# Kernel optimization log

Hardware: AMD Instinct MI355X
Metric: run time of the kernel (lower is better)

The kernel has to match this reference:

```python
import jax, jax.numpy as jnp
import numpy as np

NUM_NODES = 100000
NUM_CLASS = 63  # output channels = num_class + 1 = 64
NUM_EDGES = 1600000


def setup_inputs() -> dict:
    key = jax.random.key(0)
    k1, k2, k3, k4 = jax.random.split(key, 4)
    edges = jax.random.randint(k1, (NUM_EDGES, 2), 0, NUM_NODES, dtype=jnp.int64 if jax.config.jax_enable_x64 else jnp.int32)
    weights = jax.random.uniform(k2, (NUM_EDGES,), dtype=jnp.float32)
    poss_edge = jax.random.uniform(k3, (NUM_EDGES, NUM_CLASS + 1), dtype=jnp.float32)
    # neighbour degree sums; keep away from zero for numerical sanity
    neighbours_sum = jax.random.uniform(k4, (NUM_NODES, 1), dtype=jnp.float32, minval=0.5, maxval=1.5)
    return {"edges": edges, "weights": weights, "poss_edge": poss_edge, "neighbours_sum": neighbours_sum}


def reference(edges, weights, poss_edge, neighbours_sum):
    # value = poss_edge * weights[:, None]  -> [E, C+1]
    value = poss_edge * weights[:, None]
    # scatter_add over src node index (edges[:, 0]) into [N, C+1]
    src = edges[:, 0]
    poss_node = jax.ops.segment_sum(value, src, num_segments=NUM_NODES)
    # normalize per node by neighbour weight sum ([N,1] broadcast)
    poss_node = poss_node / neighbours_sum
    return poss_node, poss_edge
```

## Files before the change

kernel.cpp:

```cpp
#include <hip/hip_runtime.h>

#define N_NODES 100000
#define N_CLASS 64
#define N_EDGES 1600000
#define CAP     64
#define OVF_MAX 1024
#define SCAN_NB 200
#define SCAN_T  256

typedef float f4 __attribute__((ext_vector_type(4)));


__global__ __launch_bounds__(256) void fillcopy_kernel(
        const int* __restrict__ edges,
        const float* __restrict__ poss_edge,
        float* __restrict__ pe_out,
        int* __restrict__ cnt,
        int* __restrict__ slots,
        int* __restrict__ ovf_cnt,
        int* __restrict__ ovf) {
    const int wave   = (blockIdx.x * blockDim.x + threadIdx.x) >> 6;
    const int lane   = threadIdx.x & 63;
    const int grp    = lane >> 4;
    const int q      = lane & 15;
    const int nwaves = (gridDim.x * blockDim.x) >> 6;
    const int2* e2   = (const int2*)edges;

    for (int base = wave * 4; base < N_EDGES; base += nwaves * 4) {
        const int e = base + grp;
        const f4 a = __builtin_nontemporal_load((const f4*)(poss_edge + (size_t)e * N_CLASS) + q);
        __builtin_nontemporal_store(a, (f4*)(pe_out + (size_t)e * N_CLASS) + q);
        if (q == 0) {
            const int src = e2[e].x;
            const int pos = atomicAdd(&cnt[src], 1);
            if (pos < CAP) {
                slots[src * CAP + pos] = e;
            } else {
                const int k = atomicAdd(ovf_cnt, 1);
                if (k < OVF_MAX) ovf[k] = e;
            }
        }
    }
}

__global__ __launch_bounds__(256) void gather_padded_kernel(
        const int* __restrict__ cnt,
        const int* __restrict__ slots,
        const float* __restrict__ weights,
        const float* __restrict__ poss_edge,
        const float* __restrict__ nsum,
        float* __restrict__ acc) {
    const int node = blockIdx.x * 4 + (threadIdx.x >> 6);
    const int lane = threadIdx.x & 63;
    const int grp  = lane >> 4;
    const int q    = lane & 15;
    if (node >= N_NODES) return;

    const int n = min(cnt[node], CAP);
    const int* ids = slots + node * CAP;

    f4 val = (f4)(0.0f);
    int j = 0;
    for (; j + 16 <= n; j += 16) {
        const int e0 = ids[j + grp];
        const int e1 = ids[j + 4 + grp];
        const int e2 = ids[j + 8 + grp];
        const int e3 = ids[j + 12 + grp];
        const float w0 = weights[e0], w1 = weights[e1];
        const float w2 = weights[e2], w3 = weights[e3];
        const f4 a0 = __builtin_nontemporal_load((const f4*)(poss_edge + (size_t)e0 * N_CLASS) + q);
        const f4 a1 = __builtin_nontemporal_load((const f4*)(poss_edge + (size_t)e1 * N_CLASS) + q);
        const f4 a2 = __builtin_nontemporal_load((const f4*)(poss_edge + (size_t)e2 * N_CLASS) + q);
        const f4 a3 = __builtin_nontemporal_load((const f4*)(poss_edge + (size_t)e3 * N_CLASS) + q);
        val += a0 * w0;
        val += a1 * w1;
        val += a2 * w2;
        val += a3 * w3;
    }
    for (; j + 4 <= n; j += 4) {
        const int e = ids[j + grp];
        const f4 a = __builtin_nontemporal_load((const f4*)(poss_edge + (size_t)e * N_CLASS) + q);
        val += a * weights[e];
    }
    if (j < n && grp < n - j) {
        const int e = ids[j + grp];
        const f4 a = __builtin_nontemporal_load((const f4*)(poss_edge + (size_t)e * N_CLASS) + q);
        val += a * weights[e];
    }

    val.x += __shfl_xor(val.x, 16); val.y += __shfl_xor(val.y, 16);
    val.z += __shfl_xor(val.z, 16); val.w += __shfl_xor(val.w, 16);
    val.x += __shfl_xor(val.x, 32); val.y += __shfl_xor(val.y, 32);
    val.z += __shfl_xor(val.z, 32); val.w += __shfl_xor(val.w, 32);

    if (grp == 0) {
        const float inv = 1.0f / nsum[node];
        f4 o = val * inv;
        *reinterpret_cast<f4*>(acc + (size_t)node * N_CLASS + q * 4) = o;
    }
}

__global__ void cleanup_kernel(const int* __restrict__ ovf_cnt, const int* __restrict__ ovf,
                               const int* __restrict__ edges,
                               const float* __restrict__ weights,
                               const float* __restrict__ poss_edge,
                               const float* __restrict__ nsum,
                               float* __restrict__ acc) {
    const int m = min(*ovf_cnt, OVF_MAX);
    for (int t = threadIdx.x; t < m * 16; t += blockDim.x) {
        const int k = t >> 4, q = t & 15;
        const int e = ovf[k];
        const int src = edges[2 * e];
        const float w = weights[e];
        const f4 a = *((const f4*)(poss_edge + (size_t)e * N_CLASS) + q);
        const float inv = 1.0f / nsum[src];
        float* base = acc + (size_t)src * N_CLASS + q * 4;
        atomicAdd(base + 0, a.x * w * inv);
        atomicAdd(base + 1, a.y * w * inv);
        atomicAdd(base + 2, a.z * w * inv);
        atomicAdd(base + 3, a.w * w * inv);
    }
}


__global__ void hist_kernel(const int* __restrict__ edges, int* __restrict__ counts) {
    const int stride = gridDim.x * blockDim.x;
    const int2* e2 = (const int2*)edges;
    for (int e = blockIdx.x * blockDim.x + threadIdx.x; e < N_EDGES; e += stride)
        atomicAdd(&counts[e2[e].x], 1);
}

__global__ void scanA_kernel(const int* __restrict__ counts, int* __restrict__ bsum) {
    __shared__ int s[SCAN_T];
    const int b = blockIdx.x, t = threadIdx.x;
    const int i0 = b * 512 + 2 * t;
    int c0 = (i0     < N_NODES) ? counts[i0]     : 0;
    int c1 = (i0 + 1 < N_NODES) ? counts[i0 + 1] : 0;
    s[t] = c0 + c1;
    __syncthreads();
    for (int d = SCAN_T / 2; d > 0; d >>= 1) {
        if (t < d) s[t] += s[t + d];
        __syncthreads();
    }
    if (t == 0) bsum[b] = s[0];
}

__global__ void scanB_kernel(int* __restrict__ bsum, int* __restrict__ offsets) {
    __shared__ int s[SCAN_T];
    const int t = threadIdx.x;
    const int v = (t < SCAN_NB) ? bsum[t] : 0;
    s[t] = v;
    __syncthreads();
    for (int d = 1; d < SCAN_T; d <<= 1) {
        int x = (t >= d) ? s[t - d] : 0;
        __syncthreads();
        s[t] += x;
        __syncthreads();
    }
    if (t < SCAN_NB) bsum[t] = s[t] - v;
    if (t == SCAN_T - 1) offsets[N_NODES] = s[t];
}

__global__ void scanC_kernel(int* __restrict__ offsets, const int* __restrict__ bsum,
                             int* __restrict__ cursor) {
    __shared__ int s[SCAN_T];
    const int b = blockIdx.x, t = threadIdx.x;
    const int i0 = b * 512 + 2 * t;
    int c0 = (i0     < N_NODES) ? offsets[i0]     : 0;
    int c1 = (i0 + 1 < N_NODES) ? offsets[i0 + 1] : 0;
    const int pair = c0 + c1;
    s[t] = pair;
    __syncthreads();
    for (int d = 1; d < SCAN_T; d <<= 1) {
        int x = (t >= d) ? s[t - d] : 0;
        __syncthreads();
        s[t] += x;
        __syncthreads();
    }
    const int excl = s[t] - pair + bsum[b];
    if (i0 < N_NODES)     { offsets[i0]     = excl;      cursor[i0]     = excl; }
    if (i0 + 1 < N_NODES) { offsets[i0 + 1] = excl + c0; cursor[i0 + 1] = excl + c0; }
}

__global__ void place_kernel(const int* __restrict__ edges,
                             int* __restrict__ cursor,
                             int* __restrict__ edge_ids) {
    const int stride = gridDim.x * blockDim.x;
    const int2* e2 = (const int2*)edges;
    for (int e = blockIdx.x * blockDim.x + threadIdx.x; e < N_EDGES; e += stride) {
        const int src = e2[e].x;
        const int pos = atomicAdd(&cursor[src], 1);
        edge_ids[pos] = e;
    }
}

__global__ __launch_bounds__(256) void gather_csr_kernel(
        const int* __restrict__ offsets,
        const int* __restrict__ edge_ids,
        const float* __restrict__ weights,
        const float* __restrict__ poss_edge,
        const float* __restrict__ nsum,
        float* __restrict__ acc,
        float* __restrict__ pe_out) {
    const int node = blockIdx.x * 4 + (threadIdx.x >> 6);
    const int lane = threadIdx.x & 63;
    const int grp  = lane >> 4;
    const int q    = lane & 15;
    if (node >= N_NODES) return;
    const int beg = offsets[node];
    const int n   = offsets[node + 1] - beg;
    const int* ids = edge_ids + beg;

    f4 val = (f4)(0.0f);
    int j = 0;
    for (; j + 4 <= n; j += 4) {
        const int e = ids[j + grp];
        const float w = weights[e];
        const f4 a = __builtin_nontemporal_load((const f4*)(poss_edge + (size_t)e * N_CLASS) + q);
        __builtin_nontemporal_store(a, (f4*)(pe_out + (size_t)e * N_CLASS) + q);
        val += a * w;
    }
    if (j < n && grp < n - j) {
        const int e = ids[j + grp];
        const float w = weights[e];
        const f4 a = __builtin_nontemporal_load((const f4*)(poss_edge + (size_t)e * N_CLASS) + q);
        __builtin_nontemporal_store(a, (f4*)(pe_out + (size_t)e * N_CLASS) + q);
        val += a * w;
    }

    val.x += __shfl_xor(val.x, 16); val.y += __shfl_xor(val.y, 16);
    val.z += __shfl_xor(val.z, 16); val.w += __shfl_xor(val.w, 16);
    val.x += __shfl_xor(val.x, 32); val.y += __shfl_xor(val.y, 32);
    val.z += __shfl_xor(val.z, 32); val.w += __shfl_xor(val.w, 32);

    if (grp == 0) {
        const float inv = 1.0f / nsum[node];
        f4 o = val * inv;
        *reinterpret_cast<f4*>(acc + (size_t)node * N_CLASS + q * 4) = o;
    }
}

__global__ void scatter_copy_kernel(const int* __restrict__ edges,
                                    const float* __restrict__ weights,
                                    const float* __restrict__ poss_edge,
                                    float* __restrict__ acc,
                                    float* __restrict__ pe_out) {
    const int total = N_EDGES * 16;
    const int stride = gridDim.x * blockDim.x;
    for (int t = blockIdx.x * blockDim.x + threadIdx.x; t < total; t += stride) {
        const int e  = t >> 4;
        const int c0 = (t & 15) << 2;
        const float4 pe = *reinterpret_cast<const float4*>(poss_edge + (size_t)e * N_CLASS + c0);
        const float  w  = weights[e];
        const int    src = edges[2 * e];
        *reinterpret_cast<float4*>(pe_out + (size_t)e * N_CLASS + c0) = pe;
        float* a = acc + (size_t)src * N_CLASS + c0;
        atomicAdd(a + 0, pe.x * w);
        atomicAdd(a + 1, pe.y * w);
        atomicAdd(a + 2, pe.z * w);
        atomicAdd(a + 3, pe.w * w);
    }
}

__global__ void divide_kernel(float* __restrict__ acc,
                              const float* __restrict__ nsum) {
    const int t = blockIdx.x * blockDim.x + threadIdx.x;
    if (t >= N_NODES * 16) return;
    const int   node = t >> 4;
    const float d    = nsum[node];
    float4 v = *reinterpret_cast<float4*>(acc + (size_t)t * 4);
    v.x /= d; v.y /= d; v.z /= d; v.w /= d;
    *reinterpret_cast<float4*>(acc + (size_t)t * 4) = v;
}

extern "C" void kernel_launch(void* const* d_in, const int* in_sizes, int n_in,
                              void* d_out, int out_size, void* d_ws, size_t ws_size,
                              hipStream_t stream) {
    const int*   edges     = (const int*)d_in[0];
    const float* weights   = (const float*)d_in[1];
    const float* poss_edge = (const float*)d_in[2];
    const float* nsum      = (const float*)d_in[3];

    float* out    = (float*)d_out;
    float* acc    = out;
    float* pe_out = out + (size_t)N_NODES * N_CLASS;

    const size_t ws_A =
        (size_t)(N_NODES + 1 + OVF_MAX + (size_t)N_NODES * CAP) * sizeof(int);
    const size_t ws_B =
        (size_t)(N_NODES + 1 + N_NODES + 256 + N_EDGES) * sizeof(int);

    if (ws_size >= ws_A) {
        int* cnt     = (int*)d_ws;
        int* ovf_cnt = cnt + N_NODES;
        int* ovf     = ovf_cnt + 1;
        int* slots   = ovf + OVF_MAX;

        (void)hipMemsetAsync(cnt, 0, (size_t)(N_NODES + 1) * sizeof(int), stream);
        fillcopy_kernel<<<8192, 256, 0, stream>>>(
            edges, poss_edge, pe_out, cnt, slots, ovf_cnt, ovf);
        gather_padded_kernel<<<(N_NODES + 3) / 4, 256, 0, stream>>>(
            cnt, slots, weights, poss_edge, nsum, acc);
        cleanup_kernel<<<1, 256, 0, stream>>>(
            ovf_cnt, ovf, edges, weights, poss_edge, nsum, acc);
    } else if (ws_size >= ws_B) {
        int* offsets  = (int*)d_ws;
        int* cursor   = offsets + (N_NODES + 1);
        int* bsum     = cursor + N_NODES;
        int* edge_ids = bsum + 256;

        (void)hipMemsetAsync(offsets, 0, (size_t)N_NODES * sizeof(int), stream);
        hist_kernel <<<2048, 256, 0, stream>>>(edges, offsets);
        scanA_kernel<<<SCAN_NB, SCAN_T, 0, stream>>>(offsets, bsum);
        scanB_kernel<<<1, SCAN_T, 0, stream>>>(bsum, offsets);
        scanC_kernel<<<SCAN_NB, SCAN_T, 0, stream>>>(offsets, bsum, cursor);
        place_kernel<<<2048, 256, 0, stream>>>(edges, cursor, edge_ids);
        gather_csr_kernel<<<(N_NODES + 3) / 4, 256, 0, stream>>>(
            offsets, edge_ids, weights, poss_edge, nsum, acc, pe_out);
    } else {
        (void)hipMemsetAsync(acc, 0, (size_t)N_NODES * N_CLASS * sizeof(float), stream);
        scatter_copy_kernel<<<8192, 256, 0, stream>>>(edges, weights, poss_edge, acc, pe_out);
        const int div_threads = N_NODES * 16;
        divide_kernel<<<(div_threads + 255) / 256, 256, 0, stream>>>(acc, nsum);
    }
}
```

Before: 276.9 us.

## Split edge processing into two halves so gathered rows stay cache-resident

Edges are processed in two halves, each with its own fill-and-copy pass and gather pass, so the poss_edge rows a gather reads (about 205 MB per half) were just streamed by the preceding copy and may still sit in the large last-level cache. Nontemporal loads become normal loads so those rows can be retained. The first gather writes partial sums and the second adds them and normalizes. The cost is two extra launches, an extra read-modify-write of the accumulator, and a smaller per-node slot capacity (36 per half), which sends more edges to the overflow path. The overflow list is still capped at 1024 entries, so heavy nodes beyond that would be dropped.

```diff
diff --git a/kernel.cpp b/kernel.cpp
--- a/kernel.cpp
+++ b/kernel.cpp
@@ -3,22 +3,23 @@
 #define N_NODES 100000
 #define N_CLASS 64
 #define N_EDGES 1600000
+#define HALF_E  800000
+#define CAP_C   36
 #define CAP     64
 #define OVF_MAX 1024
-#define SCAN_NB 200
-#define SCAN_T  256
 
 typedef float f4 __attribute__((ext_vector_type(4)));
 
 
-__global__ __launch_bounds__(256) void fillcopy_kernel(
+__global__ __launch_bounds__(256) void fillcopy_chunk_kernel(
         const int* __restrict__ edges,
         const float* __restrict__ poss_edge,
         float* __restrict__ pe_out,
         int* __restrict__ cnt,
         int* __restrict__ slots,
         int* __restrict__ ovf_cnt,
-        int* __restrict__ ovf) {
+        int* __restrict__ ovf,
+        int e_beg, int e_end) {
     const int wave   = (blockIdx.x * blockDim.x + threadIdx.x) >> 6;
     const int lane   = threadIdx.x & 63;
     const int grp    = lane >> 4;
@@ -26,15 +27,15 @@
     const int nwaves = (gridDim.x * blockDim.x) >> 6;
     const int2* e2   = (const int2*)edges;
 
-    for (int base = wave * 4; base < N_EDGES; base += nwaves * 4) {
+    for (int base = e_beg + wave * 4; base < e_end; base += nwaves * 4) {
         const int e = base + grp;
-        const f4 a = __builtin_nontemporal_load((const f4*)(poss_edge + (size_t)e * N_CLASS) + q);
+        const f4 a = *((const f4*)(poss_edge + (size_t)e * N_CLASS) + q);
         __builtin_nontemporal_store(a, (f4*)(pe_out + (size_t)e * N_CLASS) + q);
         if (q == 0) {
             const int src = e2[e].x;
             const int pos = atomicAdd(&cnt[src], 1);
-            if (pos < CAP) {
-                slots[src * CAP + pos] = e;
+            if (pos < CAP_C) {
+                slots[src * CAP_C + pos] = e;
             } else {
                 const int k = atomicAdd(ovf_cnt, 1);
                 if (k < OVF_MAX) ovf[k] = e;
@@ -43,7 +44,8 @@
     }
 }
 
-__global__ __launch_bounds__(256) void gather_padded_kernel(
+template <int FINAL>
+__global__ __launch_bounds__(256) void gather_chunk_kernel(
         const int* __restrict__ cnt,
         const int* __restrict__ slots,
         const float* __restrict__ weights,
@@ -56,35 +58,28 @@
     const int q    = lane & 15;
     if (node >= N_NODES) return;
 
-    const int n = min(cnt[node], CAP);
-    const int* ids = slots + node * CAP;
+    const int n = min(cnt[node], CAP_C);
+    const int* ids = slots + node * CAP_C;
 
     f4 val = (f4)(0.0f);
     int j = 0;
-    for (; j + 16 <= n; j += 16) {
+    for (; j + 8 <= n; j += 8) {
         const int e0 = ids[j + grp];
         const int e1 = ids[j + 4 + grp];
-        const int e2 = ids[j + 8 + grp];
-        const int e3 = ids[j + 12 + grp];
         const float w0 = weights[e0], w1 = weights[e1];
-        const float w2 = weights[e2], w3 = weights[e3];
-        const f4 a0 = __builtin_nontemporal_load((const f4*)(poss_edge + (size_t)e0 * N_CLASS) + q);
-        const f4 a1 = __builtin_nontemporal_load((const f4*)(poss_edge + (size_t)e1 * N_CLASS) + q);
-        const f4 a2 = __builtin_nontemporal_load((const f4*)(poss_edge + (size_t)e2 * N_CLASS) + q);
-        const f4 a3 = __builtin_nontemporal_load((const f4*)(poss_edge + (size_t)e3 * N_CLASS) + q);
+        const f4 a0 = *((const f4*)(poss_edge + (size_t)e0 * N_CLASS) + q);
+        const f4 a1 = *((const f4*)(poss_edge + (size_t)e1 * N_CLASS) + q);
         val += a0 * w0;
         val += a1 * w1;
-        val += a2 * w2;
-        val += a3 * w3;
     }
     for (; j + 4 <= n; j += 4) {
         const int e = ids[j + grp];
-        const f4 a = __builtin_nontemporal_load((const f4*)(poss_edge + (size_t)e * N_CLASS) + q);
+        const f4 a = *((const f4*)(poss_edge + (size_t)e * N_CLASS) + q);
         val += a * weights[e];
     }
     if (j < n && grp < n - j) {
         const int e = ids[j + grp];
-        const f4 a = __builtin_nontemporal_load((const f4*)(poss_edge + (size_t)e * N_CLASS) + q);
+        const f4 a = *((const f4*)(poss_edge + (size_t)e * N_CLASS) + q);
         val += a * weights[e];
     }
 
@@ -94,9 +89,14 @@
     val.z += __shfl_xor(val.z, 32); val.w += __shfl_xor(val.w, 32);
 
     if (grp == 0) {
-        const float inv = 1.0f / nsum[node];
-        f4 o = val * inv;
-        *reinterpret_cast<f4*>(acc + (size_t)node * N_CLASS + q * 4) = o;
+        f4* dst = (f4*)(acc + (size_t)node * N_CLASS) + q;
+        if (FINAL) {
+            const f4 prev = *dst;
+            const float inv = 1.0f / nsum[node];
+            *dst = (val + prev) * inv;
+        } else {
+            *dst = val;
+        }
     }
 }
 
@@ -122,110 +122,81 @@
     }
 }
 
-
-__global__ void hist_kernel(const int* __restrict__ edges, int* __restrict__ counts) {
-    const int stride = gridDim.x * blockDim.x;
-    const int2* e2 = (const int2*)edges;
-    for (int e = blockIdx.x * blockDim.x + threadIdx.x; e < N_EDGES; e += stride)
-        atomicAdd(&counts[e2[e].x], 1);
-}
-
-__global__ void scanA_kernel(const int* __restrict__ counts, int* __restrict__ bsum) {
-    __shared__ int s[SCAN_T];
-    const int b = blockIdx.x, t = threadIdx.x;
-    const int i0 = b * 512 + 2 * t;
-    int c0 = (i0     < N_NODES) ? counts[i0]     : 0;
-    int c1 = (i0 + 1 < N_NODES) ? counts[i0 + 1] : 0;
-    s[t] = c0 + c1;
-    __syncthreads();
-    for (int d = SCAN_T / 2; d > 0; d >>= 1) {
-        if (t < d) s[t] += s[t + d];
-        __syncthreads();
-    }
-    if (t == 0) bsum[b] = s[0];
-}
-
-__global__ void scanB_kernel(int* __restrict__ bsum, int* __restrict__ offsets) {
-    __shared__ int s[SCAN_T];
-    const int t = threadIdx.x;
-    const int v = (t < SCAN_NB) ? bsum[t] : 0;
-    s[t] = v;
-    __syncthreads();
-    for (int d = 1; d < SCAN_T; d <<= 1) {
-        int x = (t >= d) ? s[t - d] : 0;
-        __syncthreads();
-        s[t] += x;
-        __syncthreads();
-    }
-    if (t < SCAN_NB) bsum[t] = s[t] - v;
-    if (t == SCAN_T - 1) offsets[N_NODES] = s[t];
-}
-
-__global__ void scanC_kernel(int* __restrict__ offsets, const int* __restrict__ bsum,
-                             int* __restrict__ cursor) {
-    __shared__ int s[SCAN_T];
-    const int b = blockIdx.x, t = threadIdx.x;
-    const int i0 = b * 512 + 2 * t;
-    int c0 = (i0     < N_NODES) ? offsets[i0]     : 0;
-    int c1 = (i0 + 1 < N_NODES) ? offsets[i0 + 1] : 0;
-    const int pair = c0 + c1;
-    s[t] = pair;
-    __syncthreads();
-    for (int d = 1; d < SCAN_T; d <<= 1) {
-        int x = (t >= d) ? s[t - d] : 0;
-        __syncthreads();
-        s[t] += x;
-        __syncthreads();
-    }
-    const int excl = s[t] - pair + bsum[b];
-    if (i0 < N_NODES)     { offsets[i0]     = excl;      cursor[i0]     = excl; }
-    if (i0 + 1 < N_NODES) { offsets[i0 + 1] = excl + c0; cursor[i0 + 1] = excl + c0; }
-}
-
-__global__ void place_kernel(const int* __restrict__ edges,
-                             int* __restrict__ cursor,
-                             int* __restrict__ edge_ids) {
-    const int stride = gridDim.x * blockDim.x;
-    const int2* e2 = (const int2*)edges;
-    for (int e = blockIdx.x * blockDim.x + threadIdx.x; e < N_EDGES; e += stride) {
-        const int src = e2[e].x;
-        const int pos = atomicAdd(&cursor[src], 1);
-        edge_ids[pos] = e;
-    }
-}
-
-__global__ __launch_bounds__(256) void gather_csr_kernel(
-        const int* __restrict__ offsets,
-        const int* __restrict__ edge_ids,
+__global__ __launch_bounds__(256) void fillcopy_kernel(
+        const int* __restrict__ edges,
+        const float* __restrict__ poss_edge,
+        float* __restrict__ pe_out,
+        int* __restrict__ cnt,
+        int* __restrict__ slots,
+        int* __restrict__ ovf_cnt,
+        int* __restrict__ ovf) {
+    const int wave   = (blockIdx.x * blockDim.x + threadIdx.x) >> 6;
+    const int lane   = threadIdx.x & 63;
+    const int grp    = lane >> 4;
+    const int q      = lane & 15;
+    const int nwaves = (gridDim.x * blockDim.x) >> 6;
+    const int2* e2   = (const int2*)edges;
+
+    for (int base = wave * 4; base < N_EDGES; base += nwaves * 4) {
+        const int e = base + grp;
+        const f4 a = __builtin_nontemporal_load((const f4*)(poss_edge + (size_t)e * N_CLASS) + q);
+        __builtin_nontemporal_store(a, (f4*)(pe_out + (size_t)e * N_CLASS) + q);
+        if (q == 0) {
+            const int src = e2[e].x;
+            const int pos = atomicAdd(&cnt[src], 1);
+            if (pos < CAP) {
+                slots[src * CAP + pos] = e;
+            } else {
+                const int k = atomicAdd(ovf_cnt, 1);
+                if (k < OVF_MAX) ovf[k] = e;
+            }
+        }
+    }
+}
+
+__global__ __launch_bounds__(256) void gather_padded_kernel(
+        const int* __restrict__ cnt,
+        const int* __restrict__ slots,
         const float* __restrict__ weights,
         const float* __restrict__ poss_edge,
         const float* __restrict__ nsum,
-        float* __restrict__ acc,
-        float* __restrict__ pe_out) {
+        float* __restrict__ acc) {
     const int node = blockIdx.x * 4 + (threadIdx.x >> 6);
     const int lane = threadIdx.x & 63;
     const int grp  = lane >> 4;
     const int q    = lane & 15;
     if (node >= N_NODES) return;
-    const int beg = offsets[node];
-    const int n   = offsets[node + 1] - beg;
-    const int* ids = edge_ids + beg;
+
+    const int n = min(cnt[node], CAP);
+    const int* ids = slots + node * CAP;
 
     f4 val = (f4)(0.0f);
     int j = 0;
+    for (; j + 16 <= n; j += 16) {
+        const int e0 = ids[j + grp];
+        const int e1 = ids[j + 4 + grp];
+        const int e2 = ids[j + 8 + grp];
+        const int e3 = ids[j + 12 + grp];
+        const float w0 = weights[e0], w1 = weights[e1];
+        const float w2 = weights[e2], w3 = weights[e3];
+        const f4 a0 = __builtin_nontemporal_load((const f4*)(poss_edge + (size_t)e0 * N_CLASS) + q);
+        const f4 a1 = __builtin_nontemporal_load((const f4*)(poss_edge + (size_t)e1 * N_CLASS) + q);
+        const f4 a2 = __builtin_nontemporal_load((const f4*)(poss_edge + (size_t)e2 * N_CLASS) + q);
+        const f4 a3 = __builtin_nontemporal_load((const f4*)(poss_edge + (size_t)e3 * N_CLASS) + q);
+        val += a0 * w0;
+        val += a1 * w1;
+        val += a2 * w2;
+        val += a3 * w3;
+    }
     for (; j + 4 <= n; j += 4) {
         const int e = ids[j + grp];
-        const float w = weights[e];
         const f4 a = __builtin_nontemporal_load((const f4*)(poss_edge + (size_t)e * N_CLASS) + q);
-        __builtin_nontemporal_store(a, (f4*)(pe_out + (size_t)e * N_CLASS) + q);
-        val += a * w;
+        val += a * weights[e];
     }
     if (j < n && grp < n - j) {
         const int e = ids[j + grp];
-        const float w = weights[e];
         const f4 a = __builtin_nontemporal_load((const f4*)(poss_edge + (size_t)e * N_CLASS) + q);
-        __builtin_nontemporal_store(a, (f4*)(pe_out + (size_t)e * N_CLASS) + q);
-        val += a * w;
+        val += a * weights[e];
     }
 
     val.x += __shfl_xor(val.x, 16); val.y += __shfl_xor(val.y, 16);
@@ -285,12 +256,34 @@
     float* acc    = out;
     float* pe_out = out + (size_t)N_NODES * N_CLASS;
 
+    const size_t ws_chunk =
+        (size_t)(2 * N_NODES + 1 + OVF_MAX + 2 * (size_t)N_NODES * CAP_C) * sizeof(int);
     const size_t ws_A =
         (size_t)(N_NODES + 1 + OVF_MAX + (size_t)N_NODES * CAP) * sizeof(int);
-    const size_t ws_B =
-        (size_t)(N_NODES + 1 + N_NODES + 256 + N_EDGES) * sizeof(int);
-
-    if (ws_size >= ws_A) {
+
+    if (ws_size >= ws_chunk) {
+        int* cnt0    = (int*)d_ws;
+        int* cnt1    = cnt0 + N_NODES;
+        int* ovf_cnt = cnt1 + N_NODES;
+        int* ovf     = ovf_cnt + 1;
+        int* slots0  = ovf + OVF_MAX;
+        int* slots1  = slots0 + (size_t)N_NODES * CAP_C;
+
+        (void)hipMemsetAsync(cnt0, 0, (size_t)(2 * N_NODES + 1) * sizeof(int), stream);
+
+        fillcopy_chunk_kernel<<<8192, 256, 0, stream>>>(
+            edges, poss_edge, pe_out, cnt0, slots0, ovf_cnt, ovf, 0, HALF_E);
+        gather_chunk_kernel<0><<<(N_NODES + 3) / 4, 256, 0, stream>>>(
+            cnt0, slots0, weights, poss_edge, nsum, acc);
+
+        fillcopy_chunk_kernel<<<8192, 256, 0, stream>>>(
+            edges, poss_edge, pe_out, cnt1, slots1, ovf_cnt, ovf, HALF_E, N_EDGES);
+        gather_chunk_kernel<1><<<(N_NODES + 3) / 4, 256, 0, stream>>>(
+            cnt1, slots1, weights, poss_edge, nsum, acc);
+
+        cleanup_kernel<<<1, 256, 0, stream>>>(
+            ovf_cnt, ovf, edges, weights, poss_edge, nsum, acc);
+    } else if (ws_size >= ws_A) {
         int* cnt     = (int*)d_ws;
         int* ovf_cnt = cnt + N_NODES;
         int* ovf     = ovf_cnt + 1;
@@ -303,20 +296,6 @@
             cnt, slots, weights, poss_edge, nsum, acc);
         cleanup_kernel<<<1, 256, 0, stream>>>(
             ovf_cnt, ovf, edges, weights, poss_edge, nsum, acc);
-    } else if (ws_size >= ws_B) {
-        int* offsets  = (int*)d_ws;
-        int* cursor   = offsets + (N_NODES + 1);
-        int* bsum     = cursor + N_NODES;
-        int* edge_ids = bsum + 256;
-
-        (void)hipMemsetAsync(offsets, 0, (size_t)N_NODES * sizeof(int), stream);
-        hist_kernel <<<2048, 256, 0, stream>>>(edges, offsets);
-        scanA_kernel<<<SCAN_NB, SCAN_T, 0, stream>>>(offsets, bsum);
-        scanB_kernel<<<1, SCAN_T, 0, stream>>>(bsum, offsets);
-        scanC_kernel<<<SCAN_NB, SCAN_T, 0, stream>>>(offsets, bsum, cursor);
-        place_kernel<<<2048, 256, 0, stream>>>(edges, cursor, edge_ids);
-        gather_csr_kernel<<<(N_NODES + 3) / 4, 256, 0, stream>>>(
-            offsets, edge_ids, weights, poss_edge, nsum, acc, pe_out);
     } else {
         (void)hipMemsetAsync(acc, 0, (size_t)N_NODES * N_CLASS * sizeof(float), stream);
         scatter_copy_kernel<<<8192, 256, 0, stream>>>(edges, weights, poss_edge, acc, pe_out);
```

After: 288.3 us. +4.1%, slower.
